# Optimization experiments

Measured on AMD Instinct MI355X. Metric: run time of the kernel, lower is better.

## Reference

```python
import jax, jax.numpy as jnp
import numpy as np

B, N, C, H = 4, 4096, 512, 16  # batch, seq (=input_resolution), dim, num_heads


def setup_inputs() -> dict:
    key = jax.random.key(0)
    k1, k2, k3, k4 = jax.random.split(key, 4)
    x = jax.random.normal(k1, (B, N, C), jnp.float32)
    Wqk = jax.random.normal(k2, (C, 2 * C), jnp.float32) / np.sqrt(C)
    bqk = jnp.zeros((2 * C,), jnp.float32)
    lepe_w = jax.random.normal(k3, (C, 1, 3), jnp.float32) * 0.1  # depthwise conv, groups=C
    lepe_b = jnp.zeros((C,), jnp.float32)
    return {"x": x, "Wqk": Wqk, "bqk": bqk, "lepe_w": lepe_w, "lepe_b": lepe_b}


def _rope(x):
    # x: [b, n, c]; 1D RoPE over the sequence axis, k_max = c // 2 pairs.
    b, n, c = x.shape
    k_max = c // 2
    theta = 1.0 / (10000.0 ** (jnp.arange(k_max, dtype=jnp.float32) / k_max))
    ang = jnp.arange(n, dtype=jnp.float32)[:, None] * theta  # [n, k_max]
    cos, sin = jnp.cos(ang), jnp.sin(ang)
    xr, xi = x[..., 0::2], x[..., 1::2]  # consecutive (re, im) pairs
    out = jnp.stack([xr * cos - xi * sin, xr * sin + xi * cos], axis=-1)
    return out.reshape(b, n, c)


def reference(x, Wqk, bqk, lepe_w, lepe_b):
    b, n, c = x.shape
    h = H
    d = c // h
    qk = x @ Wqk + bqk  # [b, n, 2c]
    q = jax.nn.elu(qk[..., :c]) + 1.0
    k = jax.nn.elu(qk[..., c:]) + 1.0
    q_rope = _rope(q).reshape(b, n, h, d).transpose(0, 2, 1, 3)  # [b,h,n,d]
    k_rope = _rope(k).reshape(b, n, h, d).transpose(0, 2, 1, 3)
    qh = q.reshape(b, n, h, d).transpose(0, 2, 1, 3)
    kh = k.reshape(b, n, h, d).transpose(0, 2, 1, 3)
    v = x.reshape(b, n, h, d).transpose(0, 2, 1, 3)
    # normalizer z = 1 / (q . mean_n(k) + eps)
    kmean = kh.mean(axis=2)  # [b,h,d]
    z = 1.0 / (jnp.einsum('bhnd,bhd->bhn', qh, kmean) + 1e-6)  # [b,h,n]
    # kv = (k_rope^T / sqrt(n)) @ (v / sqrt(n))
    kv = jnp.einsum('bhnd,bhne->bhde', k_rope, v) / n  # [b,h,d,d]
    out = jnp.einsum('bhnd,bhde->bhne', q_rope, kv) * z[..., None]  # [b,h,n,d]
    out = out.transpose(0, 2, 1, 3).reshape(b, n, c)
    # LePE: depthwise conv1d over sequence on v (v reassembled == x)
    vt = x.transpose(0, 2, 1)  # [b, c, n]
    lepe = jax.lax.conv_general_dilated(
        vt, lepe_w, window_strides=(1,), padding=((1, 1),),
        feature_group_count=c, dimension_numbers=('NCH', 'OIH', 'NCH'))
    lepe = lepe + lepe_b[None, :, None]
    return out + lepe.transpose(0, 2, 1)
```

## Files before the change

kernel.cpp:

```cpp
#include <hip/hip_runtime.h>

typedef unsigned short u16;
typedef u16   u16x8 __attribute__((ext_vector_type(8)));
typedef short s16x8 __attribute__((ext_vector_type(8)));
typedef float f32x4 __attribute__((ext_vector_type(4)));

__device__ __forceinline__ float b2f(u16 u) {
    return __uint_as_float(((unsigned)u) << 16);
}
__device__ __forceinline__ u16 f2b(float f) {
    unsigned x = __float_as_uint(f);
    x += 0x7fffu + ((x >> 16) & 1u);
    return (u16)(x >> 16);
}
__device__ __forceinline__ void gload_lds(const u16* g, u16* l) {
    __builtin_amdgcn_global_load_lds(
        (const __attribute__((address_space(1))) unsigned int*)g,
        (__attribute__((address_space(3))) unsigned int*)l, 16, 0, 0);
}

#define THETA_SCALE 0.05190512648261f

__global__ __launch_bounds__(256)
void k_prep(const float* __restrict__ X, u16* __restrict__ Xb,
            const float* __restrict__ W, u16* __restrict__ WT,
            float* __restrict__ kvz) {
    if (blockIdx.x < 4096) {
        size_t i = (size_t)(blockIdx.x * 256 + threadIdx.x) * 8;
        float4 a = *(const float4*)(X + i);
        float4 b = *(const float4*)(X + i + 4);
        u16x8 r;
        r[0] = f2b(a.x); r[1] = f2b(a.y); r[2] = f2b(a.z); r[3] = f2b(a.w);
        r[4] = f2b(b.x); r[5] = f2b(b.y); r[6] = f2b(b.z); r[7] = f2b(b.w);
        *(u16x8*)(Xb + i) = r;
    } else if (blockIdx.x < 4608) {
        __shared__ float tile[32][33];
        int bid = blockIdx.x - 4096;
        int c0 = (bid & 31) * 32;
        int r0 = (bid >> 5) * 32;
        int tx = threadIdx.x & 31;
        int ty = threadIdx.x >> 5;
        #pragma unroll
        for (int i = 0; i < 4; ++i) {
            int r = ty + i * 8;
            tile[r][tx] = W[(size_t)(r0 + r) * 1024 + c0 + tx];
        }
        __syncthreads();
        #pragma unroll
        for (int i = 0; i < 4; ++i) {
            int r = ty + i * 8;
            WT[(size_t)(c0 + r) * 512 + r0 + tx] = f2b(tile[tx][r]);
        }
    } else {
        size_t i = (size_t)(blockIdx.x - 4608) * 1024 + threadIdx.x * 4;
        *(float4*)(kvz + i) = make_float4(0.f, 0.f, 0.f, 0.f);
    }
}

__global__ __launch_bounds__(512, 2)
void k_gemm(const u16* __restrict__ Xb, const u16* __restrict__ WT,
            const float* __restrict__ bqk,
            u16* __restrict__ Qb, u16* __restrict__ Kb) {
    __shared__ u16 As[2][256 * 64];
    __shared__ u16 Bs[2][256 * 64];
    const int t = threadIdx.x;
    const int m0 = blockIdx.x * 256;
    const int n0 = blockIdx.y * 256;
    const int lane = t & 63;
    const int wave = t >> 6;
    const int wm = (wave >> 2) * 128;
    const int wn = (wave & 3) * 64;
    const int quad = lane >> 4;
    const int l16 = lane & 15;
    const int srow = lane >> 3;
    const int skc  = lane & 7;

    f32x4 acc[8][4];
    #pragma unroll
    for (int i = 0; i < 8; ++i)
        #pragma unroll
        for (int j = 0; j < 4; ++j) acc[i][j] = (f32x4){0.f, 0.f, 0.f, 0.f};

    #pragma unroll
    for (int c = 0; c < 4; ++c) {
        int row = c * 64 + wave * 8 + srow;
        int kcs = (skc ^ (row & 7)) * 8;
        gload_lds(Xb + (size_t)(m0 + row) * 512 + kcs,
                  &As[0][(c * 64 + wave * 8) * 64]);
        gload_lds(WT + (size_t)(n0 + row) * 512 + kcs,
                  &Bs[0][(c * 64 + wave * 8) * 64]);
    }

    for (int kt = 0; kt < 8; ++kt) {
        const int cur = kt & 1;
        if (kt < 7) {
            const int k0 = (kt + 1) * 64;
            #pragma unroll
            for (int c = 0; c < 4; ++c) {
                int row = c * 64 + wave * 8 + srow;
                int kcs = (skc ^ (row & 7)) * 8;
                gload_lds(Xb + (size_t)(m0 + row) * 512 + k0 + kcs,
                          &As[cur ^ 1][(c * 64 + wave * 8) * 64]);
                gload_lds(WT + (size_t)(n0 + row) * 512 + k0 + kcs,
                          &Bs[cur ^ 1][(c * 64 + wave * 8) * 64]);
            }
            asm volatile("s_waitcnt vmcnt(8)" ::: "memory");
        } else {
            asm volatile("s_waitcnt vmcnt(0)" ::: "memory");
        }
        __builtin_amdgcn_s_barrier();
        asm volatile("" ::: "memory");

        #pragma unroll
        for (int s = 0; s < 2; ++s) {
            const int cb = s * 4 + quad;
            s16x8 af[8], bf[4];
            #pragma unroll
            for (int f = 0; f < 8; ++f) {
                int row = wm + f * 16 + l16;
                af[f] = *(const s16x8*)&As[cur][row * 64 + ((cb ^ (row & 7)) * 8)];
            }
            #pragma unroll
            for (int j = 0; j < 4; ++j) {
                int row = wn + j * 16 + l16;
                bf[j] = *(const s16x8*)&Bs[cur][row * 64 + ((cb ^ (row & 7)) * 8)];
            }
            __builtin_amdgcn_s_setprio(1);
            #pragma unroll
            for (int f = 0; f < 8; ++f)
                #pragma unroll
                for (int j = 0; j < 4; ++j)
                    acc[f][j] = __builtin_amdgcn_mfma_f32_16x16x32_bf16(
                        af[f], bf[j], acc[f][j], 0, 0, 0);
            __builtin_amdgcn_s_setprio(0);
        }
        asm volatile("" ::: "memory");
        __builtin_amdgcn_s_barrier();
    }

    u16* O = (n0 < 512) ? Qb : Kb;
    #pragma unroll
    for (int f = 0; f < 8; ++f)
        #pragma unroll
        for (int j = 0; j < 4; ++j) {
            int col = n0 + wn + j * 16 + l16;
            float bias = bqk[col];
            int gc = col & 511;
            #pragma unroll
            for (int r = 0; r < 4; ++r) {
                int grow = m0 + wm + f * 16 + quad * 4 + r;
                float v = acc[f][j][r] + bias;
                v = v > 0.f ? v + 1.f : __expf(v);
                O[(size_t)grow * 512 + gc] = f2b(v);
            }
        }
}

__global__ __launch_bounds__(256)
void k_kv(const u16* __restrict__ Kb, const u16* __restrict__ Xb,
          float* __restrict__ kvbuf, float* __restrict__ ksum) {
    const int bh = blockIdx.x;
    const int b = bh >> 4, h = bh & 15;
    const int nb = blockIdx.y * 512;
    __shared__ u16 krT[32 * 72];
    __shared__ u16 vT[32 * 72];
    __shared__ float red[64 * 36];
    const int t = threadIdx.x;
    const int row = t >> 2;
    const int c8 = (t & 3) * 8;
    const int rot_w = 16 * ((c8 >> 3) & 3);
    const int lane = t & 63;
    const int wave = t >> 6;
    const int quad = lane >> 4;
    const int l16 = lane & 15;
    const int dq = (wave >> 1) * 16;
    const int eq = (wave & 1) * 16;
    const int ca = dq + l16;
    const int cb2 = eq + l16;
    const int rot_a = 16 * ((ca >> 3) & 3);
    const int rot_b = 16 * ((cb2 >> 3) & 3);

    float ksl[8] = {0, 0, 0, 0, 0, 0, 0, 0};
    f32x4 acc = {0.f, 0.f, 0.f, 0.f};

    float th[4];
    #pragma unroll
    for (int p = 0; p < 4; ++p)
        th[p] = exp2f(-THETA_SCALE * (float)(h * 16 + (c8 >> 1) + p));

    for (int pass = 0; pass < 8; ++pass) {
        int n = nb + pass * 64 + row;
        size_t base = (size_t)(b * 4096 + n) * 512 + h * 32 + c8;
        u16x8 k8 = *(const u16x8*)(Kb + base);
        u16x8 v8 = *(const u16x8*)(Xb + base);
        float kf[8], kr[8];
        #pragma unroll
        for (int j = 0; j < 8; ++j) kf[j] = b2f(k8[j]);
        #pragma unroll
        for (int p = 0; p < 4; ++p) {
            float sv, cv;
            sincosf((float)n * th[p], &sv, &cv);
            kr[2 * p]     = kf[2 * p] * cv - kf[2 * p + 1] * sv;
            kr[2 * p + 1] = kf[2 * p] * sv + kf[2 * p + 1] * cv;
        }
        #pragma unroll
        for (int j = 0; j < 8; ++j) ksl[j] += kf[j];
        if (pass) __syncthreads();
        int colw = (row + rot_w) & 63;
        #pragma unroll
        for (int j = 0; j < 8; ++j) {
            krT[(c8 + j) * 72 + colw] = f2b(kr[j]);
            vT[(c8 + j) * 72 + colw] = v8[j];
        }
        __syncthreads();
        #pragma unroll
        for (int ks = 0; ks < 64; ks += 32) {
            s16x8 a4 = *(const s16x8*)&krT[ca * 72 + ((ks + quad * 8 + rot_a) & 63)];
            s16x8 b4 = *(const s16x8*)&vT[cb2 * 72 + ((ks + quad * 8 + rot_b) & 63)];
            acc = __builtin_amdgcn_mfma_f32_16x16x32_bf16(a4, b4, acc, 0, 0, 0);
        }
    }

    #pragma unroll
    for (int r = 0; r < 4; ++r)
        atomicAdd(&kvbuf[(size_t)bh * 1024 + (dq + quad * 4 + r) * 32 + eq + l16],
                  acc[r]);

    __syncthreads();
    *(float4*)&red[row * 36 + c8]     = make_float4(ksl[0], ksl[1], ksl[2], ksl[3]);
    *(float4*)&red[row * 36 + c8 + 4] = make_float4(ksl[4], ksl[5], ksl[6], ksl[7]);
    __syncthreads();
    if (t < 32) {
        float s = 0.f;
        for (int r = 0; r < 64; ++r) s += red[r * 36 + t];
        atomicAdd(&ksum[bh * 32 + t], s);
    }
}

__global__ __launch_bounds__(256)
void k_out(const u16* __restrict__ Qb, const u16* __restrict__ Xb,
           const float* __restrict__ kvbuf, const float* __restrict__ ksum,
           const float* __restrict__ lw, const float* __restrict__ lb,
           float* __restrict__ OUT) {
    const int b = blockIdx.x >> 6;
    const int nb = (blockIdx.x & 63) * 64;
    const int hbase = blockIdx.y * 4;
    __shared__ u16 kvT_s[32 * 36];
    __shared__ u16 qr_s[64 * 36];
    __shared__ float out_s[64 * 36];
    __shared__ float ks_s[32];
    __shared__ float z_s[64];
    const int t = threadIdx.x;
    const int row = t >> 2;
    const int c4 = t & 3;
    const int e0 = c4 * 8;
    const int lane = t & 63;
    const int wave = t >> 6;
    const int quad = lane >> 4;
    const int l16 = lane & 15;
    const float invN = 1.f / 4096.f;
    const int n = nb + row;
    const size_t rowbase = (size_t)(b * 4096 + n) * 512;

    for (int hh = 0; hh < 4; ++hh) {
        const int h = hbase + hh;
        const int bh = b * 16 + h;
        if (hh) __syncthreads();
        {
            int id = t * 4;
            float4 kvv = *(const float4*)&kvbuf[(size_t)bh * 1024 + id];
            int d = id >> 5, e = id & 31;
            kvT_s[(e + 0) * 36 + d] = f2b(kvv.x * invN);
            kvT_s[(e + 1) * 36 + d] = f2b(kvv.y * invN);
            kvT_s[(e + 2) * 36 + d] = f2b(kvv.z * invN);
            kvT_s[(e + 3) * 36 + d] = f2b(kvv.w * invN);
        }
        if (t < 32) ks_s[t] = ksum[bh * 32 + t] * invN;
        __syncthreads();

        u16x8 q8 = *(const u16x8*)(Qb + rowbase + h * 32 + e0);
        float qf[8];
        #pragma unroll
        for (int j = 0; j < 8; ++j) qf[j] = b2f(q8[j]);
        float part = 0.f;
        #pragma unroll
        for (int j = 0; j < 8; ++j) part += qf[j] * ks_s[e0 + j];
        u16x8 qr8;
        #pragma unroll
        for (int p = 0; p < 4; ++p) {
            float th = exp2f(-THETA_SCALE * (float)(h * 16 + c4 * 4 + p));
            float sv, cv;
            sincosf((float)n * th, &sv, &cv);
            qr8[2 * p]     = f2b(qf[2 * p] * cv - qf[2 * p + 1] * sv);
            qr8[2 * p + 1] = f2b(qf[2 * p] * sv + qf[2 * p + 1] * cv);
        }
        *(u16x8*)&qr_s[row * 36 + e0] = qr8;
        part += __shfl_xor(part, 1);
        part += __shfl_xor(part, 2);
        if (c4 == 0) z_s[row] = 1.f / (part + 1e-6f);
        __syncthreads();

        {
            f32x4 zero4 = {0.f, 0.f, 0.f, 0.f};
            s16x8 a4 = *(const s16x8*)&qr_s[(wave * 16 + l16) * 36 + quad * 8];
            #pragma unroll
            for (int et = 0; et < 2; ++et) {
                s16x8 b4 = *(const s16x8*)&kvT_s[(et * 16 + l16) * 36 + quad * 8];
                f32x4 cacc = __builtin_amdgcn_mfma_f32_16x16x32_bf16(
                    a4, b4, zero4, 0, 0, 0);
                #pragma unroll
                for (int r = 0; r < 4; ++r)
                    out_s[(wave * 16 + quad * 4 + r) * 36 + et * 16 + l16] = cacc[r];
            }
        }
        __syncthreads();

        const float z = z_s[row];
        float4 o0 = *(const float4*)&out_s[row * 36 + e0];
        float4 o1 = *(const float4*)&out_s[row * 36 + e0 + 4];
        float o[8] = {o0.x, o0.y, o0.z, o0.w, o1.x, o1.y, o1.z, o1.w};
        const int cb = h * 32 + e0;
        u16x8 xc = *(const u16x8*)(Xb + rowbase + cb);
        u16x8 xm = {0, 0, 0, 0, 0, 0, 0, 0};
        u16x8 xp = {0, 0, 0, 0, 0, 0, 0, 0};
        if (n > 0)    xm = *(const u16x8*)(Xb + rowbase - 512 + cb);
        if (n < 4095) xp = *(const u16x8*)(Xb + rowbase + 512 + cb);
        float rv[8];
        #pragma unroll
        for (int j = 0; j < 8; ++j) {
            int c = cb + j;
            float lep = b2f(xm[j]) * lw[c * 3] +
                        b2f(xc[j]) * lw[c * 3 + 1] +
                        b2f(xp[j]) * lw[c * 3 + 2] + lb[c];
            rv[j] = o[j] * z + lep;
        }
        float* Of = OUT + rowbase + cb;
        *(float4*)Of       = make_float4(rv[0], rv[1], rv[2], rv[3]);
        *(float4*)(Of + 4) = make_float4(rv[4], rv[5], rv[6], rv[7]);
    }
}

extern "C" void kernel_launch(void* const* d_in, const int* in_sizes, int n_in,
                              void* d_out, int out_size, void* d_ws, size_t ws_size,
                              hipStream_t stream) {
    const float* x   = (const float*)d_in[0];
    const float* Wqk = (const float*)d_in[1];
    const float* bqk = (const float*)d_in[2];
    const float* lw  = (const float*)d_in[3];
    const float* lb  = (const float*)d_in[4];
    float* out = (float*)d_out;

    char* w = (char*)d_ws;
    u16* Kb      = (u16*)w;   w += (size_t)16384 * 512 * 2;
    u16* Qb      = (u16*)w;   w += (size_t)16384 * 512 * 2;
    u16* Xb      = (u16*)w;   w += (size_t)16384 * 512 * 2;
    u16* WT      = (u16*)w;   w += (size_t)1024 * 512 * 2;
    float* kvbuf = (float*)w; w += (size_t)64 * 1024 * 4;
    float* ksum  = (float*)w;

    k_prep<<<4674, 256, 0, stream>>>(x, Xb, Wqk, WT, kvbuf);
    k_gemm<<<dim3(64, 4), 512, 0, stream>>>(Xb, WT, bqk, Qb, Kb);
    k_kv<<<dim3(64, 8), 256, 0, stream>>>(Kb, Xb, kvbuf, ksum);
    k_out<<<dim3(256, 4), 256, 0, stream>>>(Qb, Xb, kvbuf, ksum, lw, lb, out);
}
```

Before: 141.1 us.

## Fuse K RoPE, k-sum and KV accumulation into the QK GEMM epilogue

The K half of the GEMM no longer writes K to global memory. Its epilogue applies ELU+1, accumulates the per-channel k sums, applies RoPE using an incremental sincos recurrence, then transposes K and V into shared memory and computes the per-head KV products with MFMA, adding them into kvbuf atomically. This removes the k_kv launch and the global round trip of the K tensor. In exchange the K blocks run a longer epilogue with extra barriers, a larger shared-memory footprint that may limit occupancy, and more atomics, and the recurrence may lose some RoPE accuracy.

```diff
diff --git a/kernel.cpp b/kernel.cpp
--- a/kernel.cpp
+++ b/kernel.cpp
@@ -60,9 +60,10 @@
 __global__ __launch_bounds__(512, 2)
 void k_gemm(const u16* __restrict__ Xb, const u16* __restrict__ WT,
             const float* __restrict__ bqk,
-            u16* __restrict__ Qb, u16* __restrict__ Kb) {
-    __shared__ u16 As[2][256 * 64];
-    __shared__ u16 Bs[2][256 * 64];
+            u16* __restrict__ Qb,
+            float* __restrict__ kvbuf, float* __restrict__ ksum) {
+    __shared__ u16 SM[67584];
+    __shared__ float ksum_s[256];
     const int t = threadIdx.x;
     const int m0 = blockIdx.x * 256;
     const int n0 = blockIdx.y * 256;
@@ -75,6 +76,9 @@
     const int srow = lane >> 3;
     const int skc  = lane & 7;
 
+    u16* As0 = SM;
+    u16* Bs0 = SM + 32768;
+
     f32x4 acc[8][4];
     #pragma unroll
     for (int i = 0; i < 8; ++i)
@@ -86,9 +90,9 @@
         int row = c * 64 + wave * 8 + srow;
         int kcs = (skc ^ (row & 7)) * 8;
         gload_lds(Xb + (size_t)(m0 + row) * 512 + kcs,
-                  &As[0][(c * 64 + wave * 8) * 64]);
+                  As0 + (c * 64 + wave * 8) * 64);
         gload_lds(WT + (size_t)(n0 + row) * 512 + kcs,
-                  &Bs[0][(c * 64 + wave * 8) * 64]);
+                  Bs0 + (c * 64 + wave * 8) * 64);
     }
 
     for (int kt = 0; kt < 8; ++kt) {
@@ -100,9 +104,9 @@
                 int row = c * 64 + wave * 8 + srow;
                 int kcs = (skc ^ (row & 7)) * 8;
                 gload_lds(Xb + (size_t)(m0 + row) * 512 + k0 + kcs,
-                          &As[cur ^ 1][(c * 64 + wave * 8) * 64]);
+                          As0 + (cur ^ 1) * 16384 + (c * 64 + wave * 8) * 64);
                 gload_lds(WT + (size_t)(n0 + row) * 512 + k0 + kcs,
-                          &Bs[cur ^ 1][(c * 64 + wave * 8) * 64]);
+                          Bs0 + (cur ^ 1) * 16384 + (c * 64 + wave * 8) * 64);
             }
             asm volatile("s_waitcnt vmcnt(8)" ::: "memory");
         } else {
@@ -118,12 +122,14 @@
             #pragma unroll
             for (int f = 0; f < 8; ++f) {
                 int row = wm + f * 16 + l16;
-                af[f] = *(const s16x8*)&As[cur][row * 64 + ((cb ^ (row & 7)) * 8)];
+                af[f] = *(const s16x8*)&As0[cur * 16384 + row * 64 +
+                                            ((cb ^ (row & 7)) * 8)];
             }
             #pragma unroll
             for (int j = 0; j < 4; ++j) {
                 int row = wn + j * 16 + l16;
-                bf[j] = *(const s16x8*)&Bs[cur][row * 64 + ((cb ^ (row & 7)) * 8)];
+                bf[j] = *(const s16x8*)&Bs0[cur * 16384 + row * 64 +
+                                            ((cb ^ (row & 7)) * 8)];
             }
             __builtin_amdgcn_s_setprio(1);
             #pragma unroll
@@ -138,102 +144,139 @@
         __builtin_amdgcn_s_barrier();
     }
 
-    u16* O = (n0 < 512) ? Qb : Kb;
+    if (n0 < 512) {
+        #pragma unroll
+        for (int f = 0; f < 8; ++f)
+            #pragma unroll
+            for (int j = 0; j < 4; ++j) {
+                int col = n0 + wn + j * 16 + l16;
+                float bias = bqk[col];
+                #pragma unroll
+                for (int r = 0; r < 4; ++r) {
+                    int grow = m0 + wm + f * 16 + quad * 4 + r;
+                    float v = acc[f][j][r] + bias;
+                    v = v > 0.f ? v + 1.f : __expf(v);
+                    Qb[(size_t)grow * 512 + (col & 511)] = f2b(v);
+                }
+            }
+        return;
+    }
+
+    const int b = m0 >> 12;
+    float ksp[4];
     #pragma unroll
-    for (int f = 0; f < 8; ++f)
-        #pragma unroll
-        for (int j = 0; j < 4; ++j) {
-            int col = n0 + wn + j * 16 + l16;
-            float bias = bqk[col];
-            int gc = col & 511;
+    for (int j = 0; j < 4; ++j) {
+        int colg = n0 + wn + j * 16 + l16;
+        float bias = bqk[colg];
+        int pairIdx = (colg - 512) >> 1;
+        float th = exp2f(-THETA_SCALE * (float)pairIdx);
+        float s16v, c16v;
+        sincosf(16.f * th, &s16v, &c16v);
+        float cr[4], sr[4];
+        int nb0 = (m0 & 4095) + wm + quad * 4;
+        #pragma unroll
+        for (int r = 0; r < 4; ++r)
+            sincosf((float)(nb0 + r) * th, &sr[r], &cr[r]);
+        float ks_a = 0.f;
+        #pragma unroll
+        for (int f = 0; f < 8; ++f) {
             #pragma unroll
             for (int r = 0; r < 4; ++r) {
-                int grow = m0 + wm + f * 16 + quad * 4 + r;
                 float v = acc[f][j][r] + bias;
-                v = v > 0.f ? v + 1.f : __expf(v);
-                O[(size_t)grow * 512 + gc] = f2b(v);
-            }
-        }
-}
-
-__global__ __launch_bounds__(256)
-void k_kv(const u16* __restrict__ Kb, const u16* __restrict__ Xb,
-          float* __restrict__ kvbuf, float* __restrict__ ksum) {
-    const int bh = blockIdx.x;
-    const int b = bh >> 4, h = bh & 15;
-    const int nb = blockIdx.y * 512;
-    __shared__ u16 krT[32 * 72];
-    __shared__ u16 vT[32 * 72];
-    __shared__ float red[64 * 36];
-    const int t = threadIdx.x;
-    const int row = t >> 2;
-    const int c8 = (t & 3) * 8;
-    const int rot_w = 16 * ((c8 >> 3) & 3);
-    const int lane = t & 63;
-    const int wave = t >> 6;
-    const int quad = lane >> 4;
-    const int l16 = lane & 15;
-    const int dq = (wave >> 1) * 16;
-    const int eq = (wave & 1) * 16;
-    const int ca = dq + l16;
-    const int cb2 = eq + l16;
-    const int rot_a = 16 * ((ca >> 3) & 3);
-    const int rot_b = 16 * ((cb2 >> 3) & 3);
-
-    float ksl[8] = {0, 0, 0, 0, 0, 0, 0, 0};
-    f32x4 acc = {0.f, 0.f, 0.f, 0.f};
-
-    float th[4];
+                float kf = v > 0.f ? v + 1.f : __expf(v);
+                ks_a += kf;
+                float kp = __shfl_xor(kf, 1);
+                float c = cr[r], s = sr[r];
+                acc[f][j][r] = (l16 & 1) ? (kp * s + kf * c)
+                                         : (kf * c - kp * s);
+            }
+            #pragma unroll
+            for (int r = 0; r < 4; ++r) {
+                float c = cr[r], s = sr[r];
+                cr[r] = c * c16v - s * s16v;
+                sr[r] = s * c16v + c * s16v;
+            }
+        }
+        ksp[j] = ks_a;
+    }
+    if (t < 256) ksum_s[t] = 0.f;
+    __syncthreads();
     #pragma unroll
-    for (int p = 0; p < 4; ++p)
-        th[p] = exp2f(-THETA_SCALE * (float)(h * 16 + (c8 >> 1) + p));
-
-    for (int pass = 0; pass < 8; ++pass) {
-        int n = nb + pass * 64 + row;
-        size_t base = (size_t)(b * 4096 + n) * 512 + h * 32 + c8;
-        u16x8 k8 = *(const u16x8*)(Kb + base);
-        u16x8 v8 = *(const u16x8*)(Xb + base);
-        float kf[8], kr[8];
-        #pragma unroll
-        for (int j = 0; j < 8; ++j) kf[j] = b2f(k8[j]);
-        #pragma unroll
-        for (int p = 0; p < 4; ++p) {
-            float sv, cv;
-            sincosf((float)n * th[p], &sv, &cv);
-            kr[2 * p]     = kf[2 * p] * cv - kf[2 * p + 1] * sv;
-            kr[2 * p + 1] = kf[2 * p] * sv + kf[2 * p + 1] * cv;
-        }
-        #pragma unroll
-        for (int j = 0; j < 8; ++j) ksl[j] += kf[j];
-        if (pass) __syncthreads();
-        int colw = (row + rot_w) & 63;
-        #pragma unroll
-        for (int j = 0; j < 8; ++j) {
-            krT[(c8 + j) * 72 + colw] = f2b(kr[j]);
-            vT[(c8 + j) * 72 + colw] = v8[j];
-        }
+    for (int j = 0; j < 4; ++j) {
+        float v = ksp[j];
+        v += __shfl_xor(v, 16);
+        v += __shfl_xor(v, 32);
+        if (quad == 0) atomicAdd(&ksum_s[wn + j * 16 + l16], v);
+    }
+
+    u16* krTb = SM;
+    u16* vTb  = SM + 33792;
+    const int mypass = wn >> 7;
+
+    for (int p = 0; p < 2; ++p) {
+        if (p) __syncthreads();
+        if (mypass == p) {
+            #pragma unroll
+            for (int j = 0; j < 4; ++j) {
+                int chL = (wn & 127) + j * 16 + l16;
+                int rot = 16 * ((chL >> 3) & 3);
+                #pragma unroll
+                for (int f = 0; f < 8; ++f)
+                    #pragma unroll
+                    for (int r = 0; r < 4; ++r) {
+                        int nloc = wm + f * 16 + quad * 4 + r;
+                        krTb[chL * 264 + ((nloc + rot) & 255)] =
+                            f2b(acc[f][j][r]);
+                    }
+            }
+        }
+        #pragma unroll
+        for (int cg = 0; cg < 4; ++cg)
+            #pragma unroll
+            for (int nh = 0; nh < 2; ++nh) {
+                int nloc = nh * 128 + (t >> 2);
+                int ch8 = cg * 32 + (t & 3) * 8;
+                int chg = (n0 - 512) + p * 128 + ch8;
+                u16x8 v8 = *(const u16x8*)(Xb +
+                            (size_t)(m0 + nloc) * 512 + chg);
+                #pragma unroll
+                for (int jj = 0; jj < 8; ++jj) {
+                    int chL = ch8 + jj;
+                    int rot = 16 * ((chL >> 3) & 3);
+                    vTb[chL * 264 + ((nloc + rot) & 255)] = v8[jj];
+                }
+            }
         __syncthreads();
         #pragma unroll
-        for (int ks = 0; ks < 64; ks += 32) {
-            s16x8 a4 = *(const s16x8*)&krT[ca * 72 + ((ks + quad * 8 + rot_a) & 63)];
-            s16x8 b4 = *(const s16x8*)&vT[cb2 * 72 + ((ks + quad * 8 + rot_b) & 63)];
-            acc = __builtin_amdgcn_mfma_f32_16x16x32_bf16(a4, b4, acc, 0, 0, 0);
-        }
-    }
-
-    #pragma unroll
-    for (int r = 0; r < 4; ++r)
-        atomicAdd(&kvbuf[(size_t)bh * 1024 + (dq + quad * 4 + r) * 32 + eq + l16],
-                  acc[r]);
-
-    __syncthreads();
-    *(float4*)&red[row * 36 + c8]     = make_float4(ksl[0], ksl[1], ksl[2], ksl[3]);
-    *(float4*)&red[row * 36 + c8 + 4] = make_float4(ksl[4], ksl[5], ksl[6], ksl[7]);
-    __syncthreads();
-    if (t < 32) {
-        float s = 0.f;
-        for (int r = 0; r < 64; ++r) s += red[r * 36 + t];
-        atomicAdd(&ksum[bh * 32 + t], s);
+        for (int uu = 0; uu < 2; ++uu) {
+            int u = wave + uu * 8;
+            int hl = u >> 2;
+            int dt = (u >> 1) & 1;
+            int et = u & 1;
+            int ca = hl * 32 + dt * 16 + l16;
+            int cb = hl * 32 + et * 16 + l16;
+            int ra = 16 * ((ca >> 3) & 3);
+            int rb = 16 * ((cb >> 3) & 3);
+            f32x4 a = {0.f, 0.f, 0.f, 0.f};
+            #pragma unroll
+            for (int ks = 0; ks < 8; ++ks) {
+                s16x8 av = *(const s16x8*)&krTb[ca * 264 +
+                            ((ks * 32 + quad * 8 + ra) & 255)];
+                s16x8 bv = *(const s16x8*)&vTb[cb * 264 +
+                            ((ks * 32 + quad * 8 + rb) & 255)];
+                a = __builtin_amdgcn_mfma_f32_16x16x32_bf16(av, bv, a, 0, 0, 0);
+            }
+            int H = ((n0 - 512) >> 5) + p * 4 + hl;
+            float* dst = kvbuf + (size_t)(b * 16 + H) * 1024;
+            #pragma unroll
+            for (int r = 0; r < 4; ++r)
+                atomicAdd(&dst[(dt * 16 + quad * 4 + r) * 32 + et * 16 + l16],
+                          a[r]);
+        }
+    }
+    if (t < 256) {
+        int chg = (n0 - 512) + t;
+        atomicAdd(&ksum[b * 512 + chg], ksum_s[t]);
     }
 }
 
@@ -351,7 +394,6 @@
     float* out = (float*)d_out;
 
     char* w = (char*)d_ws;
-    u16* Kb      = (u16*)w;   w += (size_t)16384 * 512 * 2;
     u16* Qb      = (u16*)w;   w += (size_t)16384 * 512 * 2;
     u16* Xb      = (u16*)w;   w += (size_t)16384 * 512 * 2;
     u16* WT      = (u16*)w;   w += (size_t)1024 * 512 * 2;
@@ -359,7 +401,6 @@
     float* ksum  = (float*)w;
 
     k_prep<<<4674, 256, 0, stream>>>(x, Xb, Wqk, WT, kvbuf);
-    k_gemm<<<dim3(64, 4), 512, 0, stream>>>(Xb, WT, bqk, Qb, Kb);
-    k_kv<<<dim3(64, 8), 256, 0, stream>>>(Kb, Xb, kvbuf, ksum);
+    k_gemm<<<dim3(64, 4), 512, 0, stream>>>(Xb, WT, bqk, Qb, kvbuf, ksum);
     k_out<<<dim3(256, 4), 256, 0, stream>>>(Qb, Xb, kvbuf, ksum, lw, lb, out);
 }
```

After: 185.4 us. 31.4% more time.
